# Performance work log

Hardware: AMD Instinct MI355X
Metric: run time of the kernel (lower is better)

## Reference

```python
import jax, jax.numpy as jnp
import numpy as np
import math

E = 2048        # embed_dim
H = 16          # num_heads
HD = E // H // 2  # head_dim = 64
DEPTH = 12
LAMBDA_INIT = 0.8 - 0.6 * math.exp(-0.3 * DEPTH)


def setup_inputs() -> dict:
    key = jax.random.key(0)
    ks = jax.random.split(key, 9)
    s = 0.02
    return {
        "x": jax.random.normal(ks[0], (2, 2048, E), jnp.float32),
        "Wq": jax.random.normal(ks[1], (E, E), jnp.float32) * s,
        "Wk": jax.random.normal(ks[2], (E, E), jnp.float32) * s,  # n_rep = 1
        "Wv": jax.random.normal(ks[3], (E, E), jnp.float32) * s,
        "Wo": jax.random.normal(ks[4], (E, E), jnp.float32) * s,
        "lq1": jax.random.normal(ks[5], (HD,), jnp.float32) * 0.1,
        "lk1": jax.random.normal(ks[6], (HD,), jnp.float32) * 0.1,
        "lq2": jax.random.normal(ks[7], (HD,), jnp.float32) * 0.1,
        "lk2": jax.random.normal(ks[8], (HD,), jnp.float32) * 0.1,
    }


def reference(x, Wq, Wk, Wv, Wo, lq1, lk1, lq2, lk2):
    b, t, e = x.shape
    scaling = HD ** (-0.5)
    # projections; split into 2*H sub-heads of dim HD for q/k, H heads of 2*HD for v
    q = (x @ Wq).reshape(b, t, 2 * H, HD).transpose(0, 2, 1, 3) * scaling  # [b,2H,t,hd]
    k = (x @ Wk).reshape(b, t, 2 * H, HD).transpose(0, 2, 1, 3)           # [b,2H,t,hd]
    v = (x @ Wv).reshape(b, t, H, 2 * HD).transpose(0, 2, 1, 3)           # [b,H,t,2hd]

    scores = jnp.einsum('bhqd,bhkd->bhqk', q, k)  # [b,2H,t,t]
    causal = jnp.triu(jnp.full((t, t), -jnp.inf, dtype=jnp.float32), 1)
    aw = jax.nn.softmax((scores + causal).astype(jnp.float32), axis=-1)

    lam = (jnp.exp(jnp.sum(lq1 * lk1)) - jnp.exp(jnp.sum(lq2 * lk2)) + LAMBDA_INIT)
    aw = aw.reshape(b, H, 2, t, t)
    aw = aw[:, :, 0] - lam * aw[:, :, 1]  # differential attention

    attn = jnp.einsum('bhqk,bhkd->bhqd', aw, v)  # [b,H,t,2hd]
    # RMSNorm over last dim (no affine), eps=1e-5
    attn = attn * jax.lax.rsqrt(jnp.mean(attn * attn, axis=-1, keepdims=True) + 1e-5)
    attn = attn * (1.0 - LAMBDA_INIT)
    attn = attn.transpose(0, 2, 1, 3).reshape(b, t, H * 2 * HD)
    return attn @ Wo
```

## Files before the change

kernel.cpp:

```cpp
#include <hip/hip_runtime.h>
#include <stdint.h>

typedef __bf16 bf16_t;
typedef __bf16 bf16x8 __attribute__((ext_vector_type(8)));
typedef __bf16 bf16x4 __attribute__((ext_vector_type(4)));
typedef float  f32x4  __attribute__((ext_vector_type(4)));
typedef float  f32x16 __attribute__((ext_vector_type(16)));
typedef unsigned int u32;

#define L2E 1.44269504088896340736f
#define LAMBDA_INIT 0.7836057665316245f
#define ONE_MINUS_LAMBDA_INIT 0.2163942334683755f

__device__ __forceinline__ void gload_lds16(const void* g, void* l) {
  __builtin_amdgcn_global_load_lds(
      (const __attribute__((address_space(1))) char*)(uintptr_t)g,
      (__attribute__((address_space(3))) char*)(uintptr_t)l, 16, 0, 0);
}

__device__ __forceinline__ f32x4 mfma_bf16(bf16x8 a, bf16x8 b, f32x4 c) {
  return __builtin_amdgcn_mfma_f32_16x16x32_bf16(a, b, c, 0, 0, 0);
}
__device__ __forceinline__ f32x16 mfma32(bf16x8 a, bf16x8 b, f32x16 c) {
  return __builtin_amdgcn_mfma_f32_32x32x16_bf16(a, b, c, 0, 0, 0);
}

__device__ __forceinline__ u32 pkbf(float a, float b) {
  union { bf16_t h[2]; u32 u; } x;
  x.h[0] = (bf16_t)a; x.h[1] = (bf16_t)b;
  return x.u;
}
__device__ __forceinline__ void pl32swap(u32& a, u32& b) {
  asm volatile("v_permlane32_swap_b32 %0, %1" : "+v"(a), "+v"(b));
}

__global__ __launch_bounds__(256) void cvt_bf16(const float* __restrict__ in,
                                                bf16_t* __restrict__ out) {
  const size_t idx = ((size_t)blockIdx.x * 256 + threadIdx.x) * 8;
  float4 a = *(const float4*)(in + idx);
  float4 c = *(const float4*)(in + idx + 4);
  bf16x8 v;
  v[0] = (bf16_t)a.x; v[1] = (bf16_t)a.y; v[2] = (bf16_t)a.z; v[3] = (bf16_t)a.w;
  v[4] = (bf16_t)c.x; v[5] = (bf16_t)c.y; v[6] = (bf16_t)c.z; v[7] = (bf16_t)c.w;
  *(bf16x8*)(out + idx) = v;
}

struct WArgs {
  const float* W[4];
  bf16_t* WT[4];
  float sc[4];
};

__global__ __launch_bounds__(256) void cvt_wT_all(WArgs a) {
  __shared__ float t[64][65];
  const int i = blockIdx.z;
  const float* W = a.W[i];
  bf16_t* WT = a.WT[i];
  const float scale = a.sc[i];
  const int k0 = blockIdx.x * 64, n0 = blockIdx.y * 64;
  const int r = threadIdx.x >> 2, cg = threadIdx.x & 3;
#pragma unroll
  for (int q = 0; q < 4; ++q) {
    float4 v = *(const float4*)(W + (size_t)(k0 + r) * 2048 + n0 + cg * 16 + q * 4);
    t[r][cg * 16 + q * 4 + 0] = v.x;
    t[r][cg * 16 + q * 4 + 1] = v.y;
    t[r][cg * 16 + q * 4 + 2] = v.z;
    t[r][cg * 16 + q * 4 + 3] = v.w;
  }
  __syncthreads();
  bf16x8 o0, o1;
#pragma unroll
  for (int j = 0; j < 8; ++j) o0[j] = (bf16_t)(t[cg * 16 + j][r] * scale);
#pragma unroll
  for (int j = 0; j < 8; ++j) o1[j] = (bf16_t)(t[cg * 16 + 8 + j][r] * scale);
  bf16_t* dst = WT + (size_t)(n0 + r) * 2048 + k0 + cg * 16;
  *(bf16x8*)dst = o0;
  *(bf16x8*)(dst + 8) = o1;
}

__global__ void lam_kernel(const float* lq1, const float* lk1,
                           const float* lq2, const float* lk2, float* out) {
  const int l = threadIdx.x;
  float p1 = lq1[l] * lk1[l];
  float p2 = lq2[l] * lk2[l];
#pragma unroll
  for (int d = 1; d < 64; d <<= 1) {
    p1 += __shfl_xor(p1, d);
    p2 += __shfl_xor(p2, d);
  }
  if (l == 0) *out = expf(p1) - expf(p2) + LAMBDA_INIT;
}

template <int OUTMODE>
__global__ __launch_bounds__(256, 2) void gemm_bt(const bf16_t* __restrict__ A,
                                                  const bf16_t* __restrict__ Bt,
                                                  void* __restrict__ Cv) {
  __shared__ __align__(16) bf16_t As[128 * 64];
  __shared__ __align__(16) bf16_t Bs[128 * 64];
  const int tid = threadIdx.x;
  const int w = tid >> 6, lane = tid & 63;
  const int wr = w >> 1, wc = w & 1;
  const int lm = lane >> 4, ln = lane & 15;
  const int nwg = (int)(gridDim.x * gridDim.y);
  const int flat = (int)blockIdx.y * (int)gridDim.x + (int)blockIdx.x;
  const int swz = (flat & 7) * (nwg >> 3) + (flat >> 3);
  const int m0 = (swz & 31) * 128, n0 = (swz >> 5) * 128;

  const f32x4 vzero = {0.f, 0.f, 0.f, 0.f};
  f32x4 acc[4][4];
#pragma unroll
  for (int m = 0; m < 4; ++m)
#pragma unroll
    for (int n = 0; n < 4; ++n) acc[m][n] = vzero;

  for (int k0 = 0; k0 < 2048; k0 += 64) {
    __syncthreads();
#pragma unroll
    for (int j = 0; j < 4; ++j) {
      const int inst = w * 4 + j;
      const int row = inst * 8 + (lane >> 3);
      const int cb = ((lane & 7) * 16) ^ ((row & 7) << 4);
      gload_lds16(A + (size_t)(m0 + row) * 2048 + k0 + (cb >> 1),
                  (char*)As + inst * 1024);
      gload_lds16(Bt + (size_t)(n0 + row) * 2048 + k0 + (cb >> 1),
                  (char*)Bs + inst * 1024);
    }
    asm volatile("s_waitcnt vmcnt(0)" ::: "memory");
    __syncthreads();

#pragma unroll
    for (int kc = 0; kc < 2; ++kc) {
      bf16x8 af[4], bfr[4];
#pragma unroll
      for (int m = 0; m < 4; ++m) {
        const int row = wr * 64 + m * 16 + ln;
        int off = row * 128 + kc * 64 + lm * 16;
        off ^= (row & 7) << 4;
        af[m] = *(const bf16x8*)((const char*)As + off);
      }
#pragma unroll
      for (int n = 0; n < 4; ++n) {
        const int row = wc * 64 + n * 16 + ln;
        int off = row * 128 + kc * 64 + lm * 16;
        off ^= (row & 7) << 4;
        bfr[n] = *(const bf16x8*)((const char*)Bs + off);
      }
      __builtin_amdgcn_s_setprio(1);
#pragma unroll
      for (int m = 0; m < 4; ++m)
#pragma unroll
        for (int n = 0; n < 4; ++n) acc[m][n] = mfma_bf16(af[m], bfr[n], acc[m][n]);
      __builtin_amdgcn_s_setprio(0);
    }
  }

  if (OUTMODE == 1) {
    bf16_t* C = (bf16_t*)Cv;
#pragma unroll
    for (int m = 0; m < 4; ++m) {
      const int growb = m0 + wr * 64 + m * 16 + lm * 4;
      const int bb = growb >> 11, t = growb & 2047;
      const int kt = t >> 6, kk = (t >> 4) & 3, hi2 = (t >> 3) & 1, e0 = t & 7;
#pragma unroll
      for (int n = 0; n < 4; ++n) {
        const int gcol = n0 + wc * 64 + n * 16 + ln;
        const int hh = gcol >> 7, g = (gcol >> 5) & 3, l31o = gcol & 31;
        bf16x4 v;
#pragma unroll
        for (int r = 0; r < 4; ++r) v[r] = (bf16_t)acc[m][n][r];
        const size_t idx = ((size_t)((bb * 16 + hh) * 32 + kt)) * 8192 +
                           (size_t)(((g * 4 + kk) * 64 + hi2 * 32 + l31o) * 8 + e0);
        *(bf16x4*)(C + idx) = v;
      }
    }
  } else if (OUTMODE == 2) {
    float* C = (float*)Cv;
#pragma unroll
    for (int m = 0; m < 4; ++m)
#pragma unroll
      for (int n = 0; n < 4; ++n)
#pragma unroll
        for (int r = 0; r < 4; ++r) {
          const size_t grow = m0 + wr * 64 + m * 16 + lm * 4 + r;
          const int gcol = n0 + wc * 64 + n * 16 + ln;
          C[grow * 2048 + gcol] = acc[m][n][r];
        }
  } else {
    bf16_t* C = (bf16_t*)Cv + ((size_t)(n0 >> 11)) * (4096u * 2048u);
#pragma unroll
    for (int m = 0; m < 4; ++m)
#pragma unroll
      for (int n = 0; n < 4; ++n)
#pragma unroll
        for (int r = 0; r < 4; ++r) {
          const size_t grow = m0 + wr * 64 + m * 16 + lm * 4 + r;
          const int gcol = (n0 + wc * 64 + n * 16 + ln) & 2047;
          C[grow * 2048 + gcol] = (bf16_t)acc[m][n][r];
        }
  }
}

__global__ __launch_bounds__(256, 2) void flash_diff(const bf16_t* __restrict__ Q,
                                                     const bf16_t* __restrict__ K,
                                                     const bf16_t* __restrict__ Vf,
                                                     bf16_t* __restrict__ attnb,
                                                     const float* __restrict__ lamP) {
  __shared__ __align__(16) char smem[65536];

  const int tid = threadIdx.x;
  const int w = tid >> 6, lane = tid & 63;
  const int qh = w >> 1, s = w & 1;
  const int l31 = lane & 31, hi = lane >> 5;

  const int bid = (int)blockIdx.x;
  const int xcd = bid & 7, p = bid >> 3;
  const int qtp = p & 15, g2 = p >> 4;
  const int hb = g2 * 8 + xcd;
  const int h = hb & 15, b = hb >> 4;
  const size_t bt0 = (size_t)b * 2048;
  const float lam = *lamP;

  auto stage_k = [&](int buf, int k0) {
#pragma unroll
    for (int j = 0; j < 4; ++j) {
      const int inst = w * 4 + j;
      const int row = inst * 4 + (lane >> 4);
      const int cb = ((lane & 15) * 16) ^ ((row & 15) << 4);
      gload_lds16(K + (bt0 + k0 + row) * 2048 + h * 128 + (cb >> 1),
                  smem + buf * 16384 + inst * 1024);
    }
  };
  auto stage_v = [&](int buf, int kt) {
    const char* src = (const char*)Vf +
                      (((size_t)((b * 16 + h) * 32 + kt)) << 14) + lane * 16;
#pragma unroll
    for (int j = 0; j < 4; ++j) {
      const int inst = w * 4 + j;
      gload_lds16(src + inst * 1024, smem + 32768 + buf * 16384 + inst * 1024);
    }
  };

  for (int half = 0; half < 2; ++half) {
    const int qt = half == 0 ? qtp : 31 - qtp;
    const int q0 = qt * 64;
    const int qloc = qh * 32 + l31;

    bf16x8 qf[4];
#pragma unroll
    for (int kc = 0; kc < 4; ++kc)
      qf[kc] = *(const bf16x8*)(Q + (bt0 + q0 + qloc) * 2048 + h * 128 +
                                s * 64 + kc * 16 + hi * 8);

    stage_k(0, 0);
    stage_v(0, 0);
    asm volatile("s_waitcnt vmcnt(0)" ::: "memory");
    __syncthreads();

    f32x16 accv[4];
#pragma unroll
    for (int m = 0; m < 4; ++m)
#pragma unroll
      for (int r = 0; r < 16; ++r) accv[m][r] = 0.f;
    float lsum = 0.f;

    int cur = 0;
    for (int kt = 0; kt <= qt; ++kt) {
      if (kt < qt) {
        stage_k(cur ^ 1, (kt + 1) * 64);
        stage_v(cur ^ 1, kt + 1);
      }
      const char* Ksb = (const char*)smem + cur * 16384;
      const char* Vsb = (const char*)smem + 32768 + cur * 16384;

      bf16x8 pf[2][2];
#pragma unroll
      for (int mt = 0; mt < 2; ++mt) {
        f32x16 sa;
#pragma unroll
        for (int r = 0; r < 16; ++r) sa[r] = 0.f;
        const int row = mt * 32 + l31;
        const int rswz = (row & 15) << 4;
        __builtin_amdgcn_s_setprio(1);
#pragma unroll
        for (int kc = 0; kc < 4; ++kc) {
          int off = row * 256 + s * 128 + kc * 32 + hi * 16;
          off ^= rswz;
          bf16x8 kf = *(const bf16x8*)(Ksb + off);
          sa = mfma32(kf, qf[kc], sa);
        }
        __builtin_amdgcn_s_setprio(0);

        if (kt == qt) {
#pragma unroll
          for (int r = 0; r < 16; ++r) {
            const int key = mt * 32 + (r & 3) + 8 * (r >> 2) + 4 * hi;
            if (key > qloc) sa[r] = -1e30f;
          }
        }
        float pv[16];
#pragma unroll
        for (int r = 0; r < 16; ++r) {
          pv[r] = exp2f(sa[r]);
          lsum += pv[r];
        }
        u32 c0 = pkbf(pv[0], pv[1]),   c1 = pkbf(pv[2], pv[3]);
        u32 c2 = pkbf(pv[4], pv[5]),   c3 = pkbf(pv[6], pv[7]);
        u32 c4 = pkbf(pv[8], pv[9]),   c5 = pkbf(pv[10], pv[11]);
        u32 c6 = pkbf(pv[12], pv[13]), c7 = pkbf(pv[14], pv[15]);
        pl32swap(c0, c2); pl32swap(c1, c3);
        pl32swap(c4, c6); pl32swap(c5, c7);
        union { u32 u[4]; bf16x8 v; } f0, f1;
        f0.u[0] = c0; f0.u[1] = c1; f0.u[2] = c2; f0.u[3] = c3;
        f1.u[0] = c4; f1.u[1] = c5; f1.u[2] = c6; f1.u[3] = c7;
        pf[mt][0] = f0.v;
        pf[mt][1] = f1.v;
      }

#pragma unroll
      for (int g = 0; g < 4; ++g) {
        __builtin_amdgcn_s_setprio(1);
#pragma unroll
        for (int kk = 0; kk < 4; ++kk) {
          bf16x8 vfr = *(const bf16x8*)(Vsb + (g * 4 + kk) * 1024 + lane * 16);
          accv[g] = mfma32(vfr, pf[kk >> 1][kk & 1], accv[g]);
        }
        __builtin_amdgcn_s_setprio(0);
      }

      asm volatile("s_waitcnt vmcnt(0)" ::: "memory");
      __syncthreads();
      cur ^= 1;
    }

    lsum += __shfl_xor(lsum, 32);
    const float rl = 1.0f / lsum;
    float* Obuf = (float*)smem;

    if (s == 1) {
#pragma unroll
      for (int mt4 = 0; mt4 < 4; ++mt4)
#pragma unroll
        for (int q2 = 0; q2 < 4; ++q2) {
          f32x4 v;
#pragma unroll
          for (int e = 0; e < 4; ++e) v[e] = accv[mt4][q2 * 4 + e] * rl;
          const int d = mt4 * 32 + q2 * 8 + hi * 4;
          *(f32x4*)(Obuf + (size_t)qloc * 128 + d) = v;
        }
    }
    __syncthreads();
    if (s == 0) {
      float o[4][16];
      float ss = 0.f;
#pragma unroll
      for (int mt4 = 0; mt4 < 4; ++mt4)
#pragma unroll
        for (int q2 = 0; q2 < 4; ++q2) {
          const int d = mt4 * 32 + q2 * 8 + hi * 4;
          f32x4 ov = *(const f32x4*)(Obuf + (size_t)qloc * 128 + d);
#pragma unroll
          for (int e = 0; e < 4; ++e) {
            const float v = accv[mt4][q2 * 4 + e] * rl - lam * ov[e];
            o[mt4][q2 * 4 + e] = v;
            ss += v * v;
          }
        }
      ss += __shfl_xor(ss, 32);
      const float sc = rsqrtf(ss * (1.0f / 128.f) + 1e-5f) * ONE_MINUS_LAMBDA_INIT;
      const size_t grow = bt0 + q0 + qloc;
#pragma unroll
      for (int mt4 = 0; mt4 < 4; ++mt4)
#pragma unroll
        for (int q2 = 0; q2 < 4; ++q2) {
          const int d = mt4 * 32 + q2 * 8 + hi * 4;
          bf16x4 v;
#pragma unroll
          for (int e = 0; e < 4; ++e) v[e] = (bf16_t)(o[mt4][q2 * 4 + e] * sc);
          *(bf16x4*)(attnb + grow * 2048 + h * 128 + d) = v;
        }
    }
    __syncthreads();
  }
}

extern "C" void kernel_launch(void* const* d_in, const int* in_sizes, int n_in,
                              void* d_out, int out_size, void* d_ws, size_t ws_size,
                              hipStream_t stream) {
  const float* x   = (const float*)d_in[0];
  const float* Wq  = (const float*)d_in[1];
  const float* Wk  = (const float*)d_in[2];
  const float* Wv  = (const float*)d_in[3];
  const float* Wo  = (const float*)d_in[4];
  const float* lq1 = (const float*)d_in[5];
  const float* lk1 = (const float*)d_in[6];
  const float* lq2 = (const float*)d_in[7];
  const float* lk2 = (const float*)d_in[8];

  char* ws = (char*)d_ws;
  bf16_t* xb    = (bf16_t*)(ws + 0);
  bf16_t* wqT   = (bf16_t*)(ws + 16777216);
  bf16_t* wkT   = (bf16_t*)(ws + 25165824);
  bf16_t* wvT   = (bf16_t*)(ws + 33554432);
  bf16_t* woT   = (bf16_t*)(ws + 41943040);
  bf16_t* Qb    = (bf16_t*)(ws + 50331648);
  bf16_t* Kb    = (bf16_t*)(ws + 67108864);
  bf16_t* Vfb   = (bf16_t*)(ws + 16777216);
  bf16_t* attnb = (bf16_t*)(ws + 0);
  float*  lamP  = (float*)(ws + 83886080);

  cvt_bf16<<<4096, 256, 0, stream>>>(x, xb);
  WArgs wa;
  wa.W[0] = Wq; wa.W[1] = Wk; wa.W[2] = Wv; wa.W[3] = Wo;
  wa.WT[0] = wqT; wa.WT[1] = wkT; wa.WT[2] = wvT; wa.WT[3] = woT;
  wa.sc[0] = 0.125f * L2E; wa.sc[1] = 1.0f; wa.sc[2] = 1.0f; wa.sc[3] = 1.0f;
  cvt_wT_all<<<dim3(32, 32, 4), 256, 0, stream>>>(wa);
  lam_kernel<<<1, 64, 0, stream>>>(lq1, lk1, lq2, lk2, lamP);

  gemm_bt<3><<<dim3(32, 32), 256, 0, stream>>>(xb, wqT, (void*)Qb);
  gemm_bt<1><<<dim3(32, 16), 256, 0, stream>>>(xb, wvT, (void*)Vfb);

  flash_diff<<<512, 256, 0, stream>>>(Qb, Kb, Vfb, attnb, lamP);

  gemm_bt<2><<<dim3(32, 16), 256, 0, stream>>>(attnb, woT, d_out);
}
```

Baseline: 281.5 us.

## Use 256x256-tile 8-wave GEMM with 4-stage LDS pipeline for fused QK projection

Replaces the 128x128-tile QK projection GEMM with a new 512-thread kernel that computes 256x256 output tiles from 128KB of dynamic LDS. It uses a 4-stage global-to-LDS prefetch ring, a swizzled LDS layout, split MFMA phases and s_setprio. The aim is more operand reuse per tile and less global traffic for the 4096x4096x2048 Q/K GEMM. In exchange it needs heavy LDS and register use, so occupancy drops and only 256 workgroups are launched. The Wk transpose now goes directly after Wq, so the two weights form one contiguous B matrix.

After: 263.3 us. -6.5%, faster.

```diff
diff --git a/kernel.cpp b/kernel.cpp
--- a/kernel.cpp
+++ b/kernel.cpp
@@ -89,6 +89,120 @@
     p2 += __shfl_xor(p2, d);
   }
   if (l == 0) *out = expf(p1) - expf(p2) + LAMBDA_INIT;
+}
+
+__global__ __launch_bounds__(512, 2) void gemm256(const bf16_t* __restrict__ A,
+                                                  const bf16_t* __restrict__ Bt,
+                                                  bf16_t* __restrict__ Cqk) {
+  extern __shared__ __align__(16) char sm[];
+  const int tid = threadIdx.x;
+  const int w = tid >> 6, lane = tid & 63;
+  const int wr = w >> 2, wc = w & 3;
+  const int lm = lane >> 4, ln = lane & 15;
+  const int nwg = (int)(gridDim.x * gridDim.y);
+  const int flat = (int)blockIdx.y * (int)gridDim.x + (int)blockIdx.x;
+  const int swz = (flat & 7) * (nwg >> 3) + (flat >> 3);
+  const int m0 = (swz & 15) * 256, n0 = (swz >> 4) * 256;
+
+  int aoff[8], boff[4];
+#pragma unroll
+  for (int m = 0; m < 8; ++m) {
+    const int row = wr * 128 + m * 16 + ln;
+    aoff[m] = row * 64 + ((lm * 16) ^ ((((row >> 2) ^ row) & 3) << 4));
+  }
+#pragma unroll
+  for (int n = 0; n < 4; ++n) {
+    const int row = wc * 64 + n * 16 + ln;
+    boff[n] = row * 64 + ((lm * 16) ^ ((((row >> 2) ^ row) & 3) << 4));
+  }
+
+  const bf16_t* gsrc[4];
+  int ldst[4];
+#pragma unroll
+  for (int j = 0; j < 4; ++j) {
+    const int r2 = j & 1, opB = j >> 1;
+    const int row = r2 * 128 + w * 16 + (lane >> 2);
+    const int colb = (lane & 3) * 16;
+    const int cb = colb ^ ((((row >> 2) ^ row) & 3) << 4);
+    gsrc[j] = (opB ? Bt + (size_t)(n0 + row) * 2048
+                   : A + (size_t)(m0 + row) * 2048) + (cb >> 1);
+    ldst[j] = opB * 16384 + r2 * 8192 + w * 1024;
+  }
+
+  const f32x4 vzero = {0.f, 0.f, 0.f, 0.f};
+  f32x4 acc[8][4];
+#pragma unroll
+  for (int m = 0; m < 8; ++m)
+#pragma unroll
+    for (int n = 0; n < 4; ++n) acc[m][n] = vzero;
+
+#pragma unroll
+  for (int kt = 0; kt < 3; ++kt)
+#pragma unroll
+    for (int j = 0; j < 4; ++j)
+      gload_lds16(gsrc[j] + kt * 32, sm + kt * 32768 + ldst[j]);
+  asm volatile("s_waitcnt vmcnt(8)" ::: "memory");
+  __builtin_amdgcn_s_barrier();
+
+  for (int kt = 0; kt < 64; ++kt) {
+    const char* sa = sm + (kt & 3) * 32768;
+    const char* sb = sa + 16384;
+    const int stage = kt + 3;
+    char* sd = sm + (stage & 3) * 32768;
+    bf16x8 bfr[4], af[4];
+
+#pragma unroll
+    for (int n = 0; n < 4; ++n) bfr[n] = *(const bf16x8*)(sb + boff[n]);
+#pragma unroll
+    for (int m = 0; m < 4; ++m) af[m] = *(const bf16x8*)(sa + aoff[m]);
+    if (stage < 64) {
+      gload_lds16(gsrc[0] + stage * 32, sd + ldst[0]);
+      gload_lds16(gsrc[1] + stage * 32, sd + ldst[1]);
+    }
+    __builtin_amdgcn_s_barrier();
+    __builtin_amdgcn_s_setprio(1);
+#pragma unroll
+    for (int m = 0; m < 4; ++m)
+#pragma unroll
+      for (int n = 0; n < 4; ++n) acc[m][n] = mfma_bf16(af[m], bfr[n], acc[m][n]);
+    __builtin_amdgcn_s_setprio(0);
+    __builtin_amdgcn_s_barrier();
+
+#pragma unroll
+    for (int m = 0; m < 4; ++m) af[m] = *(const bf16x8*)(sa + aoff[4 + m]);
+    if (stage < 64) {
+      gload_lds16(gsrc[2] + stage * 32, sd + ldst[2]);
+      gload_lds16(gsrc[3] + stage * 32, sd + ldst[3]);
+    }
+    __builtin_amdgcn_s_barrier();
+    __builtin_amdgcn_s_setprio(1);
+#pragma unroll
+    for (int m = 0; m < 4; ++m)
+#pragma unroll
+      for (int n = 0; n < 4; ++n)
+        acc[4 + m][n] = mfma_bf16(af[m], bfr[n], acc[4 + m][n]);
+    __builtin_amdgcn_s_setprio(0);
+    if (kt < 61) {
+      asm volatile("s_waitcnt vmcnt(8)" ::: "memory");
+    } else if (kt == 61) {
+      asm volatile("s_waitcnt vmcnt(4)" ::: "memory");
+    } else if (kt == 62) {
+      asm volatile("s_waitcnt vmcnt(0)" ::: "memory");
+    }
+    __builtin_amdgcn_s_barrier();
+  }
+
+  bf16_t* C = Cqk + (size_t)(n0 >> 11) * (4096u * 2048u);
+#pragma unroll
+  for (int m = 0; m < 8; ++m)
+#pragma unroll
+    for (int n = 0; n < 4; ++n)
+#pragma unroll
+      for (int r = 0; r < 4; ++r) {
+        const size_t grow = m0 + wr * 128 + m * 16 + lm * 4 + r;
+        const int gcol = (n0 + wc * 64 + n * 16 + ln) & 2047;
+        C[grow * 2048 + gcol] = (bf16_t)acc[m][n][r];
+      }
 }
 
 template <int OUTMODE>
@@ -173,7 +287,7 @@
         *(bf16x4*)(C + idx) = v;
       }
     }
-  } else if (OUTMODE == 2) {
+  } else {
     float* C = (float*)Cv;
 #pragma unroll
     for (int m = 0; m < 4; ++m)
@@ -184,18 +298,6 @@
           const size_t grow = m0 + wr * 64 + m * 16 + lm * 4 + r;
           const int gcol = n0 + wc * 64 + n * 16 + ln;
           C[grow * 2048 + gcol] = acc[m][n][r];
-        }
-  } else {
-    bf16_t* C = (bf16_t*)Cv + ((size_t)(n0 >> 11)) * (4096u * 2048u);
-#pragma unroll
-    for (int m = 0; m < 4; ++m)
-#pragma unroll
-      for (int n = 0; n < 4; ++n)
-#pragma unroll
-        for (int r = 0; r < 4; ++r) {
-          const size_t grow = m0 + wr * 64 + m * 16 + lm * 4 + r;
-          const int gcol = (n0 + wc * 64 + n * 16 + ln) & 2047;
-          C[grow * 2048 + gcol] = (bf16_t)acc[m][n][r];
         }
   }
 }
@@ -399,7 +501,6 @@
   char* ws = (char*)d_ws;
   bf16_t* xb    = (bf16_t*)(ws + 0);
   bf16_t* wqT   = (bf16_t*)(ws + 16777216);
-  bf16_t* wkT   = (bf16_t*)(ws + 25165824);
   bf16_t* wvT   = (bf16_t*)(ws + 33554432);
   bf16_t* woT   = (bf16_t*)(ws + 41943040);
   bf16_t* Qb    = (bf16_t*)(ws + 50331648);
@@ -408,15 +509,18 @@
   bf16_t* attnb = (bf16_t*)(ws + 0);
   float*  lamP  = (float*)(ws + 83886080);
 
+  hipFuncSetAttribute((const void*)gemm256,
+                      hipFuncAttributeMaxDynamicSharedMemorySize, 131072);
+
   cvt_bf16<<<4096, 256, 0, stream>>>(x, xb);
   WArgs wa;
   wa.W[0] = Wq; wa.W[1] = Wk; wa.W[2] = Wv; wa.W[3] = Wo;
-  wa.WT[0] = wqT; wa.WT[1] = wkT; wa.WT[2] = wvT; wa.WT[3] = woT;
+  wa.WT[0] = wqT; wa.WT[1] = wqT + 4194304; wa.WT[2] = wvT; wa.WT[3] = woT;
   wa.sc[0] = 0.125f * L2E; wa.sc[1] = 1.0f; wa.sc[2] = 1.0f; wa.sc[3] = 1.0f;
   cvt_wT_all<<<dim3(32, 32, 4), 256, 0, stream>>>(wa);
   lam_kernel<<<1, 64, 0, stream>>>(lq1, lk1, lq2, lk2, lamP);
 
-  gemm_bt<3><<<dim3(32, 32), 256, 0, stream>>>(xb, wqT, (void*)Qb);
+  gemm256<<<dim3(16, 16), 512, 131072, stream>>>(xb, wqT, Qb);
   gemm_bt<1><<<dim3(32, 16), 256, 0, stream>>>(xb, wvT, (void*)Vfb);
 
   flash_diff<<<512, 256, 0, stream>>>(Qb, Kb, Vfb, attnb, lamP);
```
